# Optimization experiments

Measured on AMD Instinct MI355X. Metric: run time of the kernel, lower is better.

Reference implementation:

```python
import jax, jax.numpy as jnp
import numpy as np

D_MODEL = 2048
N_HEADS = 16
D_HEAD = D_MODEL // N_HEADS


def setup_inputs() -> dict:
    key = jax.random.key(0)
    ks = jax.random.split(key, 9)
    s = 1.0 / np.sqrt(D_MODEL)
    x = jax.random.normal(ks[0], (2, 2048, D_MODEL), dtype=jnp.float32)
    wq = jax.random.uniform(ks[1], (D_MODEL, D_MODEL), jnp.float32, -s, s)
    wk = jax.random.uniform(ks[2], (D_MODEL, D_MODEL), jnp.float32, -s, s)
    wv = jax.random.uniform(ks[3], (D_MODEL, D_MODEL), jnp.float32, -s, s)
    wo = jax.random.uniform(ks[4], (D_MODEL, D_MODEL), jnp.float32, -s, s)
    bq = jax.random.uniform(ks[5], (D_MODEL,), jnp.float32, -s, s)
    bk = jax.random.uniform(ks[6], (D_MODEL,), jnp.float32, -s, s)
    bv = jax.random.uniform(ks[7], (D_MODEL,), jnp.float32, -s, s)
    bo = jax.random.uniform(ks[8], (D_MODEL,), jnp.float32, -s, s)
    return {"x": x, "wq": wq, "bq": bq, "wk": wk, "bk": bk,
            "wv": wv, "bv": bv, "wo": wo, "bo": bo}


def reference(x, wq, bq, wk, bk, wv, bv, wo, bo):
    b, s, _ = x.shape
    # torch Linear: y = x @ W.T + b
    q = (jnp.einsum('bsd,ed->bse', x, wq) + bq).reshape(b, s, N_HEADS, D_HEAD)
    k = (jnp.einsum('bsd,ed->bse', x, wk) + bk).reshape(b, s, N_HEADS, D_HEAD)
    v = (jnp.einsum('bsd,ed->bse', x, wv) + bv).reshape(b, s, N_HEADS, D_HEAD)
    scale = 1.0 / np.sqrt(D_HEAD).astype(np.float32)
    # [b, h, s, s] attention scores (naive full materialization, as in source)
    attn = jnp.einsum('bqhd,bkhd->bhqk', q, k) * scale
    attn = jax.nn.softmax(attn, axis=-1)
    out = jnp.einsum('bhqk,bkhd->bqhd', attn, v).reshape(b, s, D_MODEL)
    return jnp.einsum('bsd,ed->bse', out, wo) + bo
```

## Files before the change

kernel.cpp:

```cpp
#include <hip/hip_runtime.h>

#define D_MODEL 2048
#define SEQ     2048
#define NB      2
#define NH      16
#define DH      128
#define MROWS   (NB*SEQ)
#define GK      2048
#define NT      (GK/64)

typedef __bf16 bf16x8 __attribute__((ext_vector_type(8)));
typedef float  f32x4  __attribute__((ext_vector_type(4)));
typedef unsigned short ushort8 __attribute__((ext_vector_type(8)));
typedef unsigned int   u32x4   __attribute__((ext_vector_type(4)));

__device__ __forceinline__ unsigned short f2bf(float f) {
  unsigned int u = __float_as_uint(f);
  u += 0x7FFFu + ((u >> 16) & 1u);
  return (unsigned short)(u >> 16);
}

__device__ __forceinline__ unsigned int cvtpk_bf16(float lo, float hi) {
  unsigned int r;
  asm("v_cvt_pk_bf16_f32 %0, %1, %2" : "=v"(r) : "v"(lo), "v"(hi));
  return r;
}

__device__ __forceinline__ void gload16(void* lds, const void* g) {
  __builtin_amdgcn_global_load_lds(
      (__attribute__((address_space(1))) void*)(g),
      (__attribute__((address_space(3))) void*)(lds), 16, 0, 0);
}

__global__ __launch_bounds__(256) void cast_all(
    const float* __restrict__ x,
    const float* __restrict__ w0, const float* __restrict__ w1,
    const float* __restrict__ w2, const float* __restrict__ w3,
    unsigned short* __restrict__ xb, unsigned short* __restrict__ wb) {
  int gb = blockIdx.x;
  const float* src;
  unsigned short* dst;
  int i;
  if (gb < 4096) {
    src = x; dst = xb; i = gb * 256 + threadIdx.x;
  } else {
    int g2 = gb - 4096;
    int which = g2 >> 11;
    src = (which == 0) ? w0 : (which == 1) ? w1 : (which == 2) ? w2 : w3;
    dst = wb + (size_t)which * 4194304;
    i = (g2 & 2047) * 256 + threadIdx.x;
  }
  const float4* p = (const float4*)src;
  float4 a = p[2*i], b = p[2*i+1];
  ushort8 o;
  o[0]=f2bf(a.x); o[1]=f2bf(a.y); o[2]=f2bf(a.z); o[3]=f2bf(a.w);
  o[4]=f2bf(b.x); o[5]=f2bf(b.y); o[6]=f2bf(b.z); o[7]=f2bf(b.w);
  ((ushort8*)dst)[i] = o;
}

__global__ __launch_bounds__(512, 2) void gemm256(
    const unsigned short* __restrict__ A,
    const unsigned short* __restrict__ B,
    const float* __restrict__ b0, const float* __restrict__ b1,
    const float* __restrict__ b2,
    unsigned short* __restrict__ qo, unsigned short* __restrict__ ko,
    unsigned short* __restrict__ vo, float* __restrict__ fo,
    int mode, int nbnx)
{
  __shared__ char lds[3*49152];

  const int tid  = threadIdx.x;
  const int lane = tid & 63, wid = tid >> 6;
  const int la   = lane & 15, hi = lane >> 4;
  const int wm   = wid >> 2,  wn = wid & 3;

  const int xcd = (int)blockIdx.x & 7, ii = (int)blockIdx.x >> 3;
  const int bm  = ii / nbnx;
  const int bn  = xcd * nbnx + ii % nbnx;

  const unsigned short* Ab = A + (size_t)(bm*128) * GK;
  const unsigned short* Bb = B + (size_t)(bn*256) * GK;

  f32x4 acc[4][4];
  #pragma unroll
  for (int m = 0; m < 4; m++)
    #pragma unroll
    for (int n = 0; n < 4; n++) acc[m][n] = f32x4{0.f,0.f,0.f,0.f};

#define STAGE_A(slot, kt) do {                                                \
    int sb_ = (slot) * 49152;                                                 \
    _Pragma("unroll")                                                         \
    for (int j = 0; j < 2; j++) {                                             \
      int idx = j*512 + tid;                                                  \
      int row = idx >> 3;                                                     \
      int c   = (idx & 7) << 4;                                               \
      gload16(lds + sb_ + idx*16,                                             \
              Ab + (size_t)row*GK + (kt)*64 + ((c ^ ((row&7)<<4)) >> 1));     \
    }                                                                         \
  } while (0)

#define STAGE_B(slot, kt) do {                                                \
    int sb_ = (slot) * 49152;                                                 \
    _Pragma("unroll")                                                         \
    for (int j = 0; j < 4; j++) {                                             \
      int idx = j*512 + tid;                                                  \
      int row = idx >> 3;                                                     \
      int c   = (idx & 7) << 4;                                               \
      gload16(lds + sb_ + 16384 + idx*16,                                     \
              Bb + (size_t)row*GK + (kt)*64 + ((c ^ ((row&7)<<4)) >> 1));     \
    }                                                                         \
  } while (0)

  STAGE_A(0, 0); STAGE_B(0, 0);
  STAGE_A(1, 1); STAGE_B(1, 1);

  int cs = 0, ps = 2;
  const int xr = (la & 7) << 4;

  #pragma unroll 1
  for (int t = 0; t < NT; ++t) {
    if (t + 1 < NT) asm volatile("s_waitcnt vmcnt(6)" ::: "memory");
    else            asm volatile("s_waitcnt vmcnt(0)" ::: "memory");
    __builtin_amdgcn_s_barrier();

    const char* sa  = lds + cs*49152;
    const char* sbp = sa + 16384;

    bf16x8 bfr[4][2], aA[2][2];
    #pragma unroll
    for (int n = 0; n < 4; n++)
      #pragma unroll
      for (int ks = 0; ks < 2; ks++)
        bfr[n][ks] = *(const bf16x8*)(sbp + (((wn*64 + n*16 + la)*128 + ks*64 + hi*16) ^ xr));
    #pragma unroll
    for (int m = 0; m < 2; m++)
      #pragma unroll
      for (int ks = 0; ks < 2; ks++)
        aA[m][ks] = *(const bf16x8*)(sa + (((wm*64 + m*16 + la)*128 + ks*64 + hi*16) ^ xr));

    if (t + 2 < NT) STAGE_A(ps, t + 2);

    asm volatile("s_waitcnt lgkmcnt(0)" ::: "memory");
    __builtin_amdgcn_sched_barrier(0);
    __builtin_amdgcn_s_setprio(1);
    #pragma unroll
    for (int m = 0; m < 2; m++)
      #pragma unroll
      for (int n = 0; n < 4; n++)
        #pragma unroll
        for (int ks = 0; ks < 2; ks++)
          acc[m][n] = __builtin_amdgcn_mfma_f32_16x16x32_bf16(aA[m][ks], bfr[n][ks], acc[m][n], 0, 0, 0);
    __builtin_amdgcn_s_setprio(0);
    __builtin_amdgcn_s_barrier();

    bf16x8 aB[2][2];
    #pragma unroll
    for (int m = 0; m < 2; m++)
      #pragma unroll
      for (int ks = 0; ks < 2; ks++)
        aB[m][ks] = *(const bf16x8*)(sa + (((wm*64 + (m+2)*16 + la)*128 + ks*64 + hi*16) ^ xr));

    if (t + 2 < NT) STAGE_B(ps, t + 2);

    asm volatile("s_waitcnt lgkmcnt(0)" ::: "memory");
    __builtin_amdgcn_sched_barrier(0);
    __builtin_amdgcn_s_setprio(1);
    #pragma unroll
    for (int m = 0; m < 2; m++)
      #pragma unroll
      for (int n = 0; n < 4; n++)
        #pragma unroll
        for (int ks = 0; ks < 2; ks++)
          acc[m+2][n] = __builtin_amdgcn_mfma_f32_16x16x32_bf16(aB[m][ks], bfr[n][ks], acc[m+2][n], 0, 0, 0);
    __builtin_amdgcn_s_setprio(0);

    cs = cs + 1; if (cs == 3) cs = 0;
    ps = ps + 1; if (ps == 3) ps = 0;
  }
#undef STAGE_A
#undef STAGE_B

  const int row0 = bm*128 + wm*64;
  const int col0 = bn*256 + wn*64;

  if (mode == 1) {
    #pragma unroll
    for (int n = 0; n < 4; n++) {
      int col = col0 + n*16 + la;
      float bv = b0[col];
      #pragma unroll
      for (int m = 0; m < 4; m++)
        #pragma unroll
        for (int r = 0; r < 4; r++) {
          int row = row0 + m*16 + hi*4 + r;
          fo[(size_t)row*D_MODEL + col] = acc[m][n][r] + bv;
        }
    }
  } else {
    const int mat = col0 >> 11;
    const float* bp = (mat == 0) ? b0 : (mat == 1) ? b1 : b2;
    #pragma unroll
    for (int n = 0; n < 4; n++) {
      int col = col0 + n*16 + la;
      int c   = col & 2047;
      int h   = c >> 7, d = c & 127;
      float bv = bp[c];
      #pragma unroll
      for (int m = 0; m < 4; m++)
        #pragma unroll
        for (int r = 0; r < 4; r++) {
          int row = row0 + m*16 + hi*4 + r;
          int bb  = row >> 11, s = row & (SEQ-1);
          unsigned short val = f2bf(acc[m][n][r] + bv);
          if (mat == 0) {
            qo[((size_t)(bb*NH + h)*SEQ + s)*DH + d] = val;
          } else if (mat == 1) {
            size_t base = ((size_t)(bb*NH + h)*SEQ + (size_t)(s >> 6)*64)*DH;
            int boff = (((s & 63) << 8) + (d << 1)) ^ ((s & 7) << 4);
            ko[base + (boff >> 1)] = val;
          } else {
            size_t base = ((size_t)(bb*NH + h)*SEQ + (size_t)(s >> 6)*64)*DH;
            int boff = ((d << 7) + ((s & 63) << 1)) ^ ((d & 7) << 4);
            vo[base + (boff >> 1)] = val;
          }
        }
    }
  }
}

__global__ __launch_bounds__(256, 2) void attn_fwd(
    const unsigned short* __restrict__ Q,
    const unsigned short* __restrict__ Kg,
    const unsigned short* __restrict__ VTg,
    unsigned short* __restrict__ O)
{
  __shared__ unsigned short Ks [2][64*128];
  __shared__ unsigned short VTs[2][128*64];

  const int tid  = threadIdx.x;
  const int lane = tid & 63, wid = tid >> 6;
  const int la   = lane & 15, hi = lane >> 4;
  const int swz  = ((int)(blockIdx.x & 7) << 6) + ((int)blockIdx.x >> 3);
  const int bh   = swz >> 4;
  const int q0   = (swz & 15) << 7;
  const int b    = bh >> 4, h = bh & 15;

  const unsigned short* Qh = Q   + (size_t)bh * SEQ * DH;
  const unsigned short* Kh = Kg  + (size_t)bh * SEQ * DH;
  const unsigned short* Vh = VTg + (size_t)bh * SEQ * DH;

  const int qrow = q0 + wid * 32;

  bf16x8 qf[2][4];
  #pragma unroll
  for (int qi = 0; qi < 2; qi++)
    #pragma unroll
    for (int ks = 0; ks < 4; ks++)
      qf[qi][ks] = *(const bf16x8*)(Qh + (size_t)(qrow + qi*16 + la)*DH + ks*32 + hi*8);

  f32x4 o[2][8];
  float mrun[2], lrun[2];
  #pragma unroll
  for (int qi = 0; qi < 2; qi++) {
    #pragma unroll
    for (int df = 0; df < 8; df++) o[qi][df] = f32x4{0.f,0.f,0.f,0.f};
    mrun[qi] = -1e30f; lrun[qi] = 0.f;
  }

  #pragma unroll
  for (int i = 0; i < 4; i++) {
    int off = i*4096 + tid*16;
    gload16((char*)Ks[0]  + off, (const char*)Kh + off);
    gload16((char*)VTs[0] + off, (const char*)Vh + off);
  }
  __syncthreads();

  const float sc2 = 0.1275424483f;

  #pragma unroll 1
  for (int t = 0; t < SEQ/64; ++t) {
    const int cur = t & 1;

    if (t + 1 < SEQ/64) {
      const char* kt = (const char*)(Kh + (size_t)(t+1)*(64*DH));
      const char* vt = (const char*)(Vh + (size_t)(t+1)*(64*DH));
      #pragma unroll
      for (int i = 0; i < 4; i++) {
        int off = i*4096 + tid*16;
        gload16((char*)Ks[cur^1]  + off, kt + off);
        gload16((char*)VTs[cur^1] + off, vt + off);
      }
    }

    f32x4 S[4][2];
    #pragma unroll
    for (int mf = 0; mf < 4; mf++)
      #pragma unroll
      for (int qi = 0; qi < 2; qi++) S[mf][qi] = f32x4{0.f,0.f,0.f,0.f};
    #pragma unroll
    for (int ks = 0; ks < 4; ks++) {
      bf16x8 kf[4];
      #pragma unroll
      for (int mf = 0; mf < 4; mf++) {
        int boff = (((mf*16 + la) << 8) + (ks << 6) + (hi << 4)) ^ ((la & 7) << 4);
        kf[mf] = *(const bf16x8*)((const char*)Ks[cur] + boff);
      }
      #pragma unroll
      for (int mf = 0; mf < 4; mf++)
        #pragma unroll
        for (int qi = 0; qi < 2; qi++)
          S[mf][qi] = __builtin_amdgcn_mfma_f32_16x16x32_bf16(kf[mf], qf[qi][ks], S[mf][qi], 0, 0, 0);
    }

    unsigned int pf[2][2][4];
    #pragma unroll
    for (int qi = 0; qi < 2; qi++) {
      float pm = S[0][qi][0];
      #pragma unroll
      for (int mf = 0; mf < 4; mf++)
        #pragma unroll
        for (int r = 0; r < 4; r++) pm = fmaxf(pm, S[mf][qi][r]);
      pm = fmaxf(pm, __shfl_xor(pm, 16));
      pm = fmaxf(pm, __shfl_xor(pm, 32));
      pm *= sc2;

      float mn;
      if (__all(pm <= mrun[qi] + 8.0f)) {
        mn = mrun[qi];
      } else {
        mn = fmaxf(mrun[qi], pm);
        float alpha = __builtin_amdgcn_exp2f(mrun[qi] - mn);
        mrun[qi] = mn;
        lrun[qi] *= alpha;
        #pragma unroll
        for (int r = 0; r < 4; r++) {
          float ar = __shfl(alpha, (lane & 48) | ((hi << 2) | r), 64);
          #pragma unroll
          for (int df = 0; df < 8; df++) o[qi][df][r] *= ar;
        }
      }

      float p[4][4]; float rs = 0.f;
      #pragma unroll
      for (int mf = 0; mf < 4; mf++)
        #pragma unroll
        for (int r = 0; r < 4; r++) {
          float e = __builtin_amdgcn_exp2f(fmaf(S[mf][qi][r], sc2, -mn));
          p[mf][r] = e; rs += e;
        }
      rs += __shfl_xor(rs, 16);
      rs += __shfl_xor(rs, 32);
      lrun[qi] += rs;

      unsigned int c[4][2];
      #pragma unroll
      for (int mf = 0; mf < 4; mf++) {
        c[mf][0] = cvtpk_bf16(p[mf][0], p[mf][1]);
        c[mf][1] = cvtpk_bf16(p[mf][2], p[mf][3]);
      }
      #pragma unroll
      for (int ks2 = 0; ks2 < 2; ks2++) {
        #pragma unroll
        for (int w = 0; w < 4; w++) {
          int src = la + 16*(2*(hi & 1) + (w >> 1));
          unsigned int t0 = __shfl(c[2*ks2    ][w & 1], src, 64);
          unsigned int t1 = __shfl(c[2*ks2 + 1][w & 1], src, 64);
          pf[qi][ks2][w] = (hi >> 1) ? t1 : t0;
        }
      }
    }

    #pragma unroll
    for (int ks2 = 0; ks2 < 2; ks2++) {
      #pragma unroll
      for (int df = 0; df < 8; df++) {
        int vrow = df*16 + la;
        int boff = ((vrow << 7) + (ks2 << 6) + (hi << 4)) ^ ((la & 7) << 4);
        bf16x8 vf = *(const bf16x8*)((const char*)VTs[cur] + boff);
        #pragma unroll
        for (int qi = 0; qi < 2; qi++) {
          u32x4 pw = {pf[qi][ks2][0], pf[qi][ks2][1], pf[qi][ks2][2], pf[qi][ks2][3]};
          o[qi][df] = __builtin_amdgcn_mfma_f32_16x16x32_bf16(
              __builtin_bit_cast(bf16x8, pw), vf, o[qi][df], 0, 0, 0);
        }
      }
    }
    __syncthreads();
  }

  unsigned short* Ob = O + (size_t)b * SEQ * D_MODEL + h * DH;
  #pragma unroll
  for (int qi = 0; qi < 2; qi++) {
    float linv[4];
    #pragma unroll
    for (int r = 0; r < 4; r++)
      linv[r] = 1.0f / __shfl(lrun[qi], (lane & 48) | ((hi << 2) | r), 64);
    #pragma unroll
    for (int df = 0; df < 8; df++)
      #pragma unroll
      for (int r = 0; r < 4; r++) {
        int srow = qrow + qi*16 + hi*4 + r;
        Ob[(size_t)srow * D_MODEL + df*16 + la] = f2bf(o[qi][df][r] * linv[r]);
      }
  }
}

extern "C" void kernel_launch(void* const* d_in, const int* in_sizes, int n_in,
                              void* d_out, int out_size, void* d_ws, size_t ws_size,
                              hipStream_t stream) {
  const float* x  = (const float*)d_in[0];
  const float* wq = (const float*)d_in[1];
  const float* bq = (const float*)d_in[2];
  const float* wk = (const float*)d_in[3];
  const float* bk = (const float*)d_in[4];
  const float* wv = (const float*)d_in[5];
  const float* bv = (const float*)d_in[6];
  const float* wo = (const float*)d_in[7];
  const float* bo = (const float*)d_in[8];
  float* out = (float*)d_out;

  const size_t X = (size_t)MROWS * D_MODEL;
  const size_t W = (size_t)D_MODEL * D_MODEL;

  unsigned short* ws  = (unsigned short*)d_ws;
  unsigned short* xb  = ws;
  unsigned short* wqb = xb  + X;
  unsigned short* wkb = wqb + W;
  unsigned short* wvb = wkb + W;
  unsigned short* wob = wvb + W;
  unsigned short* qb  = wob + W;
  unsigned short* kb  = qb  + X;
  unsigned short* vtg = kb  + X;
  unsigned short* ab  = vtg + X;

  cast_all<<<dim3(12288), 256, 0, stream>>>(x, wq, wk, wv, wo, xb, wqb);

  gemm256<<<dim3(768), 512, 0, stream>>>(xb, wqb, bq, bk, bv,
                                         qb, kb, vtg, nullptr, 0, 3);

  attn_fwd<<<dim3(512), 256, 0, stream>>>(qb, kb, vtg, ab);

  gemm256<<<dim3(256), 512, 0, stream>>>(ab, wob, bo, bo, bo,
                                         nullptr, nullptr, nullptr, out, 1, 1);
}
```

Before: 280.3 us.

## Add dedicated 256x192-tile QKV GEMM kernel with double-buffered LDS

Adds a separate QKV projection kernel that uses 256x192 output tiles, giving 512 blocks instead of 768. These 512 blocks map exactly onto 256 CUs at two blocks per CU. It uses double-buffered LDS staging in place of triple buffering, and works out the Q/K/V bias and layout per column because a 192-wide tile can straddle matrix boundaries. The aim is to remove the partial last wave and raise per-block operand reuse. In exchange it holds more accumulator registers and has fewer stages to hide load latency. The output-projection GEMM is simplified to its single mode.

Result: no change. 276.4 us (-1.4%).

```diff
diff --git a/kernel.cpp b/kernel.cpp
--- a/kernel.cpp
+++ b/kernel.cpp
@@ -58,14 +58,155 @@
   ((ushort8*)dst)[i] = o;
 }
 
-__global__ __launch_bounds__(512, 2) void gemm256(
+__global__ __launch_bounds__(512, 2) void gemm192(
     const unsigned short* __restrict__ A,
     const unsigned short* __restrict__ B,
     const float* __restrict__ b0, const float* __restrict__ b1,
     const float* __restrict__ b2,
     unsigned short* __restrict__ qo, unsigned short* __restrict__ ko,
-    unsigned short* __restrict__ vo, float* __restrict__ fo,
-    int mode, int nbnx)
+    unsigned short* __restrict__ vo)
+{
+  __shared__ char lds[2*57344];
+
+  const int tid  = threadIdx.x;
+  const int lane = tid & 63, wid = tid >> 6;
+  const int la   = lane & 15, hi = lane >> 4;
+  const int wm   = wid >> 2,  wn = wid & 3;
+
+  const int xcd = (int)blockIdx.x & 7, ii = (int)blockIdx.x >> 3;
+  const int bm  = ii >> 2;
+  const int bn  = xcd * 4 + (ii & 3);
+
+  const unsigned short* Ab = A + (size_t)(bm*256) * GK;
+  const unsigned short* Bb = B + (size_t)(bn*192) * GK;
+
+  f32x4 acc[8][3];
+  #pragma unroll
+  for (int m = 0; m < 8; m++)
+    #pragma unroll
+    for (int n = 0; n < 3; n++) acc[m][n] = f32x4{0.f,0.f,0.f,0.f};
+
+#define STG(slot, kt) do {                                                    \
+    char* base_ = lds + (slot)*57344;                                         \
+    _Pragma("unroll")                                                         \
+    for (int j = 0; j < 4; j++) {                                             \
+      int idx = j*512 + tid;                                                  \
+      int row = idx >> 3;                                                     \
+      int c   = (idx & 7) << 4;                                               \
+      gload16(base_ + idx*16,                                                 \
+              Ab + (size_t)row*GK + (kt)*64 + ((c ^ ((row&7)<<4)) >> 1));     \
+    }                                                                         \
+    _Pragma("unroll")                                                         \
+    for (int j = 0; j < 3; j++) {                                             \
+      int idx = j*512 + tid;                                                  \
+      int row = idx >> 3;                                                     \
+      int c   = (idx & 7) << 4;                                               \
+      gload16(base_ + 32768 + idx*16,                                         \
+              Bb + (size_t)row*GK + (kt)*64 + ((c ^ ((row&7)<<4)) >> 1));     \
+    }                                                                         \
+  } while (0)
+
+  STG(0, 0);
+  const int xr = (la & 7) << 4;
+
+  #pragma unroll 1
+  for (int t = 0; t < NT; ++t) {
+    if (t + 1 < NT) {
+      STG((t+1)&1, t+1);
+      asm volatile("s_waitcnt vmcnt(7)" ::: "memory");
+    } else {
+      asm volatile("s_waitcnt vmcnt(0)" ::: "memory");
+    }
+    __builtin_amdgcn_s_barrier();
+
+    const char* sa  = lds + (t&1)*57344;
+    const char* sbp = sa + 32768;
+
+    bf16x8 bfr[3][2], aA[4][2];
+    #pragma unroll
+    for (int n = 0; n < 3; n++)
+      #pragma unroll
+      for (int ks = 0; ks < 2; ks++)
+        bfr[n][ks] = *(const bf16x8*)(sbp + (((wn*48 + n*16 + la)*128 + ks*64 + hi*16) ^ xr));
+    #pragma unroll
+    for (int m = 0; m < 4; m++)
+      #pragma unroll
+      for (int ks = 0; ks < 2; ks++)
+        aA[m][ks] = *(const bf16x8*)(sa + (((wm*128 + m*16 + la)*128 + ks*64 + hi*16) ^ xr));
+
+    asm volatile("s_waitcnt lgkmcnt(0)" ::: "memory");
+    __builtin_amdgcn_sched_barrier(0);
+    __builtin_amdgcn_s_setprio(1);
+    #pragma unroll
+    for (int m = 0; m < 4; m++)
+      #pragma unroll
+      for (int n = 0; n < 3; n++)
+        #pragma unroll
+        for (int ks = 0; ks < 2; ks++)
+          acc[m][n] = __builtin_amdgcn_mfma_f32_16x16x32_bf16(aA[m][ks], bfr[n][ks], acc[m][n], 0, 0, 0);
+    __builtin_amdgcn_s_setprio(0);
+    __builtin_amdgcn_s_barrier();
+
+    bf16x8 aB[4][2];
+    #pragma unroll
+    for (int m = 0; m < 4; m++)
+      #pragma unroll
+      for (int ks = 0; ks < 2; ks++)
+        aB[m][ks] = *(const bf16x8*)(sa + (((wm*128 + (m+4)*16 + la)*128 + ks*64 + hi*16) ^ xr));
+
+    asm volatile("s_waitcnt lgkmcnt(0)" ::: "memory");
+    __builtin_amdgcn_sched_barrier(0);
+    __builtin_amdgcn_s_setprio(1);
+    #pragma unroll
+    for (int m = 0; m < 4; m++)
+      #pragma unroll
+      for (int n = 0; n < 3; n++)
+        #pragma unroll
+        for (int ks = 0; ks < 2; ks++)
+          acc[m+4][n] = __builtin_amdgcn_mfma_f32_16x16x32_bf16(aB[m][ks], bfr[n][ks], acc[m+4][n], 0, 0, 0);
+    __builtin_amdgcn_s_setprio(0);
+    __builtin_amdgcn_s_barrier();
+  }
+#undef STG
+
+  const int row0 = bm*256 + wm*128;
+  const int col0 = bn*192 + wn*48;
+  #pragma unroll
+  for (int n = 0; n < 3; n++) {
+    int col = col0 + n*16 + la;
+    int mat = col >> 11;
+    int c   = col & 2047;
+    int h   = c >> 7, d = c & 127;
+    const float* bp = (mat == 0) ? b0 : (mat == 1) ? b1 : b2;
+    float bv = bp[c];
+    #pragma unroll
+    for (int m = 0; m < 8; m++)
+      #pragma unroll
+      for (int r = 0; r < 4; r++) {
+        int row = row0 + m*16 + hi*4 + r;
+        int bb  = row >> 11, s = row & (SEQ-1);
+        unsigned short val = f2bf(acc[m][n][r] + bv);
+        if (mat == 0) {
+          qo[((size_t)(bb*NH + h)*SEQ + s)*DH + d] = val;
+        } else if (mat == 1) {
+          size_t base = ((size_t)(bb*NH + h)*SEQ + (size_t)(s >> 6)*64)*DH;
+          int boff = (((s & 63) << 8) + (d << 1)) ^ ((s & 7) << 4);
+          ko[base + (boff >> 1)] = val;
+        } else {
+          size_t base = ((size_t)(bb*NH + h)*SEQ + (size_t)(s >> 6)*64)*DH;
+          int boff = ((d << 7) + ((s & 63) << 1)) ^ ((d & 7) << 4);
+          vo[base + (boff >> 1)] = val;
+        }
+      }
+  }
+}
+
+__global__ __launch_bounds__(512, 2) void gemm256(
+    const unsigned short* __restrict__ A,
+    const unsigned short* __restrict__ B,
+    const float* __restrict__ b0,
+    float* __restrict__ fo,
+    int nbnx)
 {
   __shared__ char lds[3*49152];
 
@@ -182,49 +323,17 @@
 
   const int row0 = bm*128 + wm*64;
   const int col0 = bn*256 + wn*64;
-
-  if (mode == 1) {
-    #pragma unroll
-    for (int n = 0; n < 4; n++) {
-      int col = col0 + n*16 + la;
-      float bv = b0[col];
-      #pragma unroll
-      for (int m = 0; m < 4; m++)
-        #pragma unroll
-        for (int r = 0; r < 4; r++) {
-          int row = row0 + m*16 + hi*4 + r;
-          fo[(size_t)row*D_MODEL + col] = acc[m][n][r] + bv;
-        }
-    }
-  } else {
-    const int mat = col0 >> 11;
-    const float* bp = (mat == 0) ? b0 : (mat == 1) ? b1 : b2;
-    #pragma unroll
-    for (int n = 0; n < 4; n++) {
-      int col = col0 + n*16 + la;
-      int c   = col & 2047;
-      int h   = c >> 7, d = c & 127;
-      float bv = bp[c];
-      #pragma unroll
-      for (int m = 0; m < 4; m++)
-        #pragma unroll
-        for (int r = 0; r < 4; r++) {
-          int row = row0 + m*16 + hi*4 + r;
-          int bb  = row >> 11, s = row & (SEQ-1);
-          unsigned short val = f2bf(acc[m][n][r] + bv);
-          if (mat == 0) {
-            qo[((size_t)(bb*NH + h)*SEQ + s)*DH + d] = val;
-          } else if (mat == 1) {
-            size_t base = ((size_t)(bb*NH + h)*SEQ + (size_t)(s >> 6)*64)*DH;
-            int boff = (((s & 63) << 8) + (d << 1)) ^ ((s & 7) << 4);
-            ko[base + (boff >> 1)] = val;
-          } else {
-            size_t base = ((size_t)(bb*NH + h)*SEQ + (size_t)(s >> 6)*64)*DH;
-            int boff = ((d << 7) + ((s & 63) << 1)) ^ ((d & 7) << 4);
-            vo[base + (boff >> 1)] = val;
-          }
-        }
-    }
+  #pragma unroll
+  for (int n = 0; n < 4; n++) {
+    int col = col0 + n*16 + la;
+    float bv = b0[col];
+    #pragma unroll
+    for (int m = 0; m < 4; m++)
+      #pragma unroll
+      for (int r = 0; r < 4; r++) {
+        int row = row0 + m*16 + hi*4 + r;
+        fo[(size_t)row*D_MODEL + col] = acc[m][n][r] + bv;
+      }
   }
 }
 
@@ -435,11 +544,9 @@
 
   cast_all<<<dim3(12288), 256, 0, stream>>>(x, wq, wk, wv, wo, xb, wqb);
 
-  gemm256<<<dim3(768), 512, 0, stream>>>(xb, wqb, bq, bk, bv,
-                                         qb, kb, vtg, nullptr, 0, 3);
+  gemm192<<<dim3(512), 512, 0, stream>>>(xb, wqb, bq, bk, bv, qb, kb, vtg);
 
   attn_fwd<<<dim3(512), 256, 0, stream>>>(qb, kb, vtg, ab);
 
-  gemm256<<<dim3(256), 512, 0, stream>>>(ab, wob, bo, bo, bo,
-                                         nullptr, nullptr, nullptr, out, 1, 1);
-}
+  gemm256<<<dim3(256), 512, 0, stream>>>(ab, wob, bo, out, 1);
+}
```
